# Kernel tuning notes

Measured on AMD Instinct MI355X. Metric: run time of the kernel, lower is better.

The kernel has to match this reference:

```python
import jax, jax.numpy as jnp
import numpy as np

N_CLS = 1000
FEAT_DIM = 1024
BATCH = 32768
PROTO_M = 0.95
TEMP = 0.1
BASE_TEMP = 0.1


def setup_inputs() -> dict:
    key = jax.random.key(0)
    k1, k2, k3 = jax.random.split(key, 3)
    features = jax.random.normal(k1, (BATCH, FEAT_DIM), dtype=jnp.float32)
    labels = jax.random.randint(k2, (BATCH,), 0, N_CLS)
    p = jax.random.normal(k3, (N_CLS, FEAT_DIM), dtype=jnp.float32)
    prototypes = p / jnp.maximum(jnp.linalg.norm(p, axis=1, keepdims=True), 1e-12)
    return {"features": features, "prototypes": prototypes, "labels": labels}


def _l2_normalize(x, eps=1e-12):
    # F.normalize(x, dim=0) semantics: x / max(||x||_2, eps)
    return x / jnp.maximum(jnp.linalg.norm(x), eps)


def _ema_update(prototypes, features, labels):
    # Sequential per-sample EMA + renormalize (faithful to the torch for-loop:
    # later samples with the same label see earlier updates).
    def step(protos, fl):
        f, l = fl
        row = _l2_normalize(protos[l] * PROTO_M + f * (1.0 - PROTO_M))
        return protos.at[l].set(row), None

    prototypes, _ = jax.lax.scan(step, prototypes, (features, labels))
    return prototypes


def reference(features, prototypes, labels):
    protos = _ema_update(prototypes, features, labels)  # [n_cls, feat]
    logits = jnp.matmul(protos, protos.T) / TEMP        # [n_cls, n_cls]
    # mask = (1 - eye) * logits_mask, where logits_mask also zeros the diagonal
    mask = 1.0 - jnp.eye(N_CLS, dtype=logits.dtype)
    mean_prob_neg = jnp.log((mask * jnp.exp(logits)).sum(axis=1) / mask.sum(axis=1))
    # torch drops NaNs; with n_cls > 1 every row has n_cls-1 negatives, so none occur
    loss = (TEMP / BASE_TEMP) * jnp.mean(mean_prob_neg)
    return loss
```

## Files before the change

### kernel.cpp

```cpp
#include <hip/hip_runtime.h>
#include <hip/hip_bf16.h>
#include <math.h>

#define N_CLS 1000
#define FEAT  1024
#define BATCH 32768
#define NBLK_H 128
#define CHUNK  256
#define KCAT   3072
#define GBK    64
#define LPITCH 72

typedef short short8 __attribute__((ext_vector_type(8)));
typedef float f32x4  __attribute__((ext_vector_type(4)));

__device__ __forceinline__ unsigned short f2bf(float x) {
    union { __hip_bfloat16 h; unsigned short u; } cv;
    cv.h = __float2bfloat16(x);
    return cv.u;
}
__device__ __forceinline__ float bf2f(unsigned short u) {
    union { __hip_bfloat16 h; unsigned short u; } cv;
    cv.u = u;
    return __bfloat162float(cv.h);
}

__global__ __launch_bounds__(256) void hist_kernel(const int* __restrict__ labels,
                                                   unsigned* __restrict__ hist) {
    __shared__ unsigned cnt[N_CLS];
    const int t = threadIdx.x, b = blockIdx.x;
    for (int i = t; i < N_CLS; i += 256) cnt[i] = 0;
    __syncthreads();
    atomicAdd(&cnt[labels[b * CHUNK + t]], 1u);
    __syncthreads();
    for (int i = t; i < N_CLS; i += 256) hist[(size_t)i * NBLK_H + b] = cnt[i];
}

__global__ __launch_bounds__(256) void scan1_kernel(unsigned* __restrict__ hist,
                                                    unsigned* __restrict__ total) {
    const int l    = blockIdx.x * 4 + (threadIdx.x >> 6);
    const int lane = threadIdx.x & 63;
    unsigned v0 = hist[(size_t)l * NBLK_H + lane];
    unsigned v1 = hist[(size_t)l * NBLK_H + 64 + lane];
    unsigned x0 = v0, x1 = v1;
    #pragma unroll
    for (int off = 1; off < 64; off <<= 1) {
        unsigned u0 = __shfl_up(x0, off, 64);
        if (lane >= off) x0 += u0;
        unsigned u1 = __shfl_up(x1, off, 64);
        if (lane >= off) x1 += u1;
    }
    x1 += __shfl(x0, 63, 64);
    hist[(size_t)l * NBLK_H + lane]      = x0 - v0;
    hist[(size_t)l * NBLK_H + 64 + lane] = x1 - v1;
    if (lane == 63) total[l] = x1;
}

__global__ __launch_bounds__(1024) void scan2_kernel(const unsigned* __restrict__ total,
                                                     unsigned* __restrict__ base) {
    const int t = threadIdx.x;
    unsigned v = (t < N_CLS) ? total[t] : 0u;
    __shared__ unsigned sc[1024];
    sc[t] = v;
    __syncthreads();
    for (int off = 1; off < 1024; off <<= 1) {
        unsigned u = (t >= off) ? sc[t - off] : 0u;
        __syncthreads();
        sc[t] += u;
        __syncthreads();
    }
    if (t < N_CLS) base[t] = sc[t] - v;
}

__global__ __launch_bounds__(256) void scatter_kernel(const int* __restrict__ labels,
                                                      const unsigned* __restrict__ hist,
                                                      const unsigned* __restrict__ base,
                                                      int* __restrict__ sorted_idx) {
    __shared__ int lbl[CHUNK];
    __shared__ unsigned c[N_CLS];
    const int t = threadIdx.x, b = blockIdx.x;
    for (int i = t; i < N_CLS; i += 256) c[i] = 0;
    __syncthreads();
    const int i = b * CHUNK + t;
    const int l = labels[i];
    lbl[t] = l;
    atomicAdd(&c[l], 1u);
    __syncthreads();
    int rank = 0;
    if (c[l] > 1) {
        for (int j = 0; j < t; ++j) rank += (lbl[j] == l);
    }
    sorted_idx[base[l] + hist[(size_t)l * NBLK_H + b] + (unsigned)rank] = i;
}

__device__ __forceinline__ float4 ema4(float4 p, float4 f) {
    p.x = fmaf(0.95f, p.x, 0.05f * f.x);
    p.y = fmaf(0.95f, p.y, 0.05f * f.y);
    p.z = fmaf(0.95f, p.z, 0.05f * f.z);
    p.w = fmaf(0.95f, p.w, 0.05f * f.w);
    return p;
}
__device__ __forceinline__ float dot4(float4 a) {
    return a.x * a.x + a.y * a.y + a.z * a.z + a.w * a.w;
}
__device__ __forceinline__ float4 scale4(float4 a, float s) {
    a.x *= s; a.y *= s; a.z *= s; a.w *= s; return a;
}

__global__ __launch_bounds__(256) void ema_kernel(const float* __restrict__ features,
                                                  const float* __restrict__ prototypes,
                                                  const int* __restrict__ sorted_idx,
                                                  const unsigned* __restrict__ base,
                                                  const unsigned* __restrict__ total,
                                                  float* __restrict__ protos_new) {
    const int w    = blockIdx.x * 4 + (threadIdx.x >> 6);
    const int lane = threadIdx.x & 63;
    const float4* pr = (const float4*)(prototypes + (size_t)w * FEAT);
    float4 p0 = pr[lane], p1 = pr[lane + 64], p2 = pr[lane + 128], p3 = pr[lane + 192];

    const int cnt = (int)total[w];
    const int bs  = (int)base[w];
    const int iA = (cnt > 0) ? sorted_idx[bs] : 0;
    const int iB = (cnt > 1) ? sorted_idx[bs + 1] : 0;
    const float4* fA = (const float4*)(features + (size_t)iA * FEAT);
    float4 a0 = fA[lane], a1 = fA[lane + 64], a2 = fA[lane + 128], a3 = fA[lane + 192];
    const float4* fB = (const float4*)(features + (size_t)iB * FEAT);
    float4 b0 = fB[lane], b1 = fB[lane + 64], b2 = fB[lane + 128], b3 = fB[lane + 192];

    int k = 0;
    while (k + 2 <= cnt) {
        {
            const int iN = (k + 2 < cnt) ? sorted_idx[bs + k + 2] : 0;
            p0 = ema4(p0, a0); p1 = ema4(p1, a1); p2 = ema4(p2, a2); p3 = ema4(p3, a3);
            const float4* f = (const float4*)(features + (size_t)iN * FEAT);
            a0 = f[lane]; a1 = f[lane + 64]; a2 = f[lane + 128]; a3 = f[lane + 192];
            float ss = dot4(p0) + dot4(p1) + dot4(p2) + dot4(p3);
            #pragma unroll
            for (int o = 32; o; o >>= 1) ss += __shfl_xor(ss, o, 64);
            const float inv = 1.0f / fmaxf(sqrtf(ss), 1e-12f);
            p0 = scale4(p0, inv); p1 = scale4(p1, inv); p2 = scale4(p2, inv); p3 = scale4(p3, inv);
        }
        {
            const int iN = (k + 3 < cnt) ? sorted_idx[bs + k + 3] : 0;
            p0 = ema4(p0, b0); p1 = ema4(p1, b1); p2 = ema4(p2, b2); p3 = ema4(p3, b3);
            const float4* f = (const float4*)(features + (size_t)iN * FEAT);
            b0 = f[lane]; b1 = f[lane + 64]; b2 = f[lane + 128]; b3 = f[lane + 192];
            float ss = dot4(p0) + dot4(p1) + dot4(p2) + dot4(p3);
            #pragma unroll
            for (int o = 32; o; o >>= 1) ss += __shfl_xor(ss, o, 64);
            const float inv = 1.0f / fmaxf(sqrtf(ss), 1e-12f);
            p0 = scale4(p0, inv); p1 = scale4(p1, inv); p2 = scale4(p2, inv); p3 = scale4(p3, inv);
        }
        k += 2;
    }
    if (k < cnt) {
        p0 = ema4(p0, a0); p1 = ema4(p1, a1); p2 = ema4(p2, a2); p3 = ema4(p3, a3);
        float ss = dot4(p0) + dot4(p1) + dot4(p2) + dot4(p3);
        #pragma unroll
        for (int o = 32; o; o >>= 1) ss += __shfl_xor(ss, o, 64);
        const float inv = 1.0f / fmaxf(sqrtf(ss), 1e-12f);
        p0 = scale4(p0, inv); p1 = scale4(p1, inv); p2 = scale4(p2, inv); p3 = scale4(p3, inv);
    }
    float4* out = (float4*)(protos_new + (size_t)w * FEAT);
    out[lane] = p0; out[lane + 64] = p1; out[lane + 128] = p2; out[lane + 192] = p3;
}

__global__ __launch_bounds__(256) void convert_kernel(const float* __restrict__ P,
                                                      unsigned short* __restrict__ A,
                                                      unsigned short* __restrict__ Bm) {
    const int row = blockIdx.x;
    const int t   = threadIdx.x;
    float4 v = make_float4(0.f, 0.f, 0.f, 0.f);
    if (row < N_CLS) v = *(const float4*)(P + (size_t)row * FEAT + 4 * t);
    ushort4 hi, lo;
    hi.x = f2bf(v.x); lo.x = f2bf(v.x - bf2f(hi.x));
    hi.y = f2bf(v.y); lo.y = f2bf(v.y - bf2f(hi.y));
    hi.z = f2bf(v.z); lo.z = f2bf(v.z - bf2f(hi.z));
    hi.w = f2bf(v.w); lo.w = f2bf(v.w - bf2f(hi.w));
    const size_t rb = (size_t)row * KCAT;
    *(ushort4*)(A  + rb +        4 * t) = hi;
    *(ushort4*)(A  + rb + 1024 + 4 * t) = lo;
    *(ushort4*)(A  + rb + 2048 + 4 * t) = hi;
    *(ushort4*)(Bm + rb +        4 * t) = hi;
    *(ushort4*)(Bm + rb + 1024 + 4 * t) = hi;
    *(ushort4*)(Bm + rb + 2048 + 4 * t) = lo;
}

__global__ __launch_bounds__(256) void gram_kernel(const unsigned short* __restrict__ A,
                                                   const unsigned short* __restrict__ Bm,
                                                   float* __restrict__ S) {
    __shared__ short As[64 * LPITCH];
    __shared__ short Bs[64 * LPITCH];
    const int t = threadIdx.x;
    const int l = t & 63, wid = t >> 6;
    const int wr = wid >> 1, wc = wid & 1;
    const int m0 = blockIdx.y * 64, n0 = blockIdx.x * 64;
    const int lg = l >> 4, lc = l & 15;

    f32x4 acc[2][2] = {};

    const int r0s = t >> 3,          c0s = t & 7;
    const int r1s = (t + 256) >> 3,  c1s = t & 7;
    const short* Ag = (const short*)A;
    const short* Bg = (const short*)Bm;

    for (int k0 = 0; k0 < KCAT; k0 += GBK) {
        short8 a0 = *(const short8*)(Ag + (size_t)(m0 + r0s) * KCAT + k0 + c0s * 8);
        short8 a1 = *(const short8*)(Ag + (size_t)(m0 + r1s) * KCAT + k0 + c1s * 8);
        short8 g0 = *(const short8*)(Bg + (size_t)(n0 + r0s) * KCAT + k0 + c0s * 8);
        short8 g1 = *(const short8*)(Bg + (size_t)(n0 + r1s) * KCAT + k0 + c1s * 8);
        __syncthreads();
        *(short8*)(As + r0s * LPITCH + c0s * 8) = a0;
        *(short8*)(As + r1s * LPITCH + c1s * 8) = a1;
        *(short8*)(Bs + r0s * LPITCH + c0s * 8) = g0;
        *(short8*)(Bs + r1s * LPITCH + c1s * 8) = g1;
        __syncthreads();
        #pragma unroll
        for (int kk = 0; kk < 2; ++kk) {
            short8 af[2], bf[2];
            #pragma unroll
            for (int mi = 0; mi < 2; ++mi)
                af[mi] = *(const short8*)(As + (wr * 32 + mi * 16 + lc) * LPITCH + kk * 32 + lg * 8);
            #pragma unroll
            for (int ni = 0; ni < 2; ++ni)
                bf[ni] = *(const short8*)(Bs + (wc * 32 + ni * 16 + lc) * LPITCH + kk * 32 + lg * 8);
            #pragma unroll
            for (int mi = 0; mi < 2; ++mi)
                #pragma unroll
                for (int ni = 0; ni < 2; ++ni)
                    acc[mi][ni] = __builtin_amdgcn_mfma_f32_16x16x32_bf16(af[mi], bf[ni], acc[mi][ni], 0, 0, 0);
        }
    }

    #pragma unroll
    for (int mi = 0; mi < 2; ++mi) {
        #pragma unroll
        for (int j = 0; j < 4; ++j) {
            const int gr = m0 + wr * 32 + mi * 16 + lg * 4 + j;
            float s = 0.f;
            #pragma unroll
            for (int ni = 0; ni < 2; ++ni) {
                const int gc = n0 + wc * 32 + ni * 16 + lc;
                if (gr < N_CLS && gc < N_CLS && gr != gc) s += expf(acc[mi][ni][j] * 10.0f);
            }
            #pragma unroll
            for (int m = 1; m < 16; m <<= 1) s += __shfl_xor(s, m, 64);
            if (lc == 0 && gr < N_CLS) atomicAdd(&S[gr], s);
        }
    }
}

__global__ __launch_bounds__(1024) void loss_kernel(const float* __restrict__ S,
                                                    float* __restrict__ out) {
    const int t = threadIdx.x;
    float v = 0.f;
    if (t < N_CLS) v = logf(S[t]) - logf(999.0f);
    #pragma unroll
    for (int off = 32; off; off >>= 1) v += __shfl_xor(v, off, 64);
    __shared__ float red[16];
    const int wv = t >> 6, lane = t & 63;
    if (lane == 0) red[wv] = v;
    __syncthreads();
    if (t < 16) {
        float s = red[t];
        #pragma unroll
        for (int off = 8; off; off >>= 1) s += __shfl_xor(s, off, 16);
        if (t == 0) out[0] = s / (float)N_CLS;
    }
}

extern "C" void kernel_launch(void* const* d_in, const int* in_sizes, int n_in,
                              void* d_out, int out_size, void* d_ws, size_t ws_size,
                              hipStream_t stream) {
    const float* features   = (const float*)d_in[0];
    const float* prototypes = (const float*)d_in[1];
    const int*   labels     = (const int*)d_in[2];
    float* out = (float*)d_out;

    char* ws = (char*)d_ws;
    unsigned*       hist   = (unsigned*)(ws);
    unsigned*       base   = (unsigned*)(ws + 0x80000);
    unsigned*       total  = (unsigned*)(ws + 0x81000);
    int*            sorted = (int*)     (ws + 0x82000);
    float*          S      = (float*)   (ws + 0xA4000);
    float*          pnew   = (float*)   (ws + 0x100000);
    unsigned short* Acat   = (unsigned short*)(ws + 0x500000);
    unsigned short* Bcat   = (unsigned short*)(ws + 0xB00000);

    hist_kernel   <<<NBLK_H, 256, 0, stream>>>(labels, hist);
    scan1_kernel  <<<250, 256, 0, stream>>>(hist, total);
    scan2_kernel  <<<1, 1024, 0, stream>>>(total, base);
    scatter_kernel<<<NBLK_H, 256, 0, stream>>>(labels, hist, base, sorted);
    hipMemsetAsync(S, 0, N_CLS * sizeof(float), stream);
    ema_kernel    <<<250, 256, 0, stream>>>(features, prototypes, sorted, base, total, pnew);
    convert_kernel<<<1024, 256, 0, stream>>>(pnew, Acat, Bcat);
    gram_kernel   <<<dim3(16, 16), 256, 0, stream>>>(Acat, Bcat, S);
    loss_kernel   <<<1, 1024, 0, stream>>>(S, out);
}
```

Measured before the change: 265.4 us.

## Fuse bf16 split into EMA, inline loss in gram, deepen feature prefetch

```diff
diff --git a/kernel.cpp b/kernel.cpp
--- a/kernel.cpp
+++ b/kernel.cpp
@@ -7,9 +7,8 @@
 #define BATCH 32768
 #define NBLK_H 128
 #define CHUNK  256
-#define KCAT   3072
-#define GBK    64
 #define LPITCH 72
+#define GRAM_BLOCKS 256
 
 typedef short short8 __attribute__((ext_vector_type(8)));
 typedef float f32x4  __attribute__((ext_vector_type(4)));
@@ -26,9 +25,15 @@
 }
 
 __global__ __launch_bounds__(256) void hist_kernel(const int* __restrict__ labels,
-                                                   unsigned* __restrict__ hist) {
+                                                   unsigned* __restrict__ hist,
+                                                   float* __restrict__ S,
+                                                   unsigned* __restrict__ counter) {
     __shared__ unsigned cnt[N_CLS];
     const int t = threadIdx.x, b = blockIdx.x;
+    if (b == 0) {
+        for (int i = t; i < N_CLS; i += 256) S[i] = 0.0f;
+        if (t == 0) *counter = 0u;
+    }
     for (int i = t; i < N_CLS; i += 256) cnt[i] = 0;
     __syncthreads();
     atomicAdd(&cnt[labels[b * CHUNK + t]], 1u);
@@ -107,12 +112,38 @@
     a.x *= s; a.y *= s; a.z *= s; a.w *= s; return a;
 }
 
+__device__ __forceinline__ void ema_step(float4& p0, float4& p1, float4& p2, float4& p3,
+                                         float4& x0, float4& x1, float4& x2, float4& x3,
+                                         const float* __restrict__ features, int iN, int lane) {
+    p0 = ema4(p0, x0); p1 = ema4(p1, x1); p2 = ema4(p2, x2); p3 = ema4(p3, x3);
+    const float4* f = (const float4*)(features + (size_t)iN * FEAT);
+    x0 = f[lane]; x1 = f[lane + 64]; x2 = f[lane + 128]; x3 = f[lane + 192];
+    float ss = dot4(p0) + dot4(p1) + dot4(p2) + dot4(p3);
+    #pragma unroll
+    for (int o = 32; o; o >>= 1) ss += __shfl_xor(ss, o, 64);
+    const float inv = 1.0f / fmaxf(sqrtf(ss), 1e-12f);
+    p0 = scale4(p0, inv); p1 = scale4(p1, inv); p2 = scale4(p2, inv); p3 = scale4(p3, inv);
+}
+
+__device__ __forceinline__ void write_hl(unsigned short* __restrict__ H,
+                                         unsigned short* __restrict__ L,
+                                         size_t off, float4 v) {
+    ushort4 hi, lo;
+    hi.x = f2bf(v.x); lo.x = f2bf(v.x - bf2f(hi.x));
+    hi.y = f2bf(v.y); lo.y = f2bf(v.y - bf2f(hi.y));
+    hi.z = f2bf(v.z); lo.z = f2bf(v.z - bf2f(hi.z));
+    hi.w = f2bf(v.w); lo.w = f2bf(v.w - bf2f(hi.w));
+    *(ushort4*)(H + off) = hi;
+    *(ushort4*)(L + off) = lo;
+}
+
 __global__ __launch_bounds__(256) void ema_kernel(const float* __restrict__ features,
                                                   const float* __restrict__ prototypes,
                                                   const int* __restrict__ sorted_idx,
                                                   const unsigned* __restrict__ base,
                                                   const unsigned* __restrict__ total,
-                                                  float* __restrict__ protos_new) {
+                                                  unsigned short* __restrict__ Hg,
+                                                  unsigned short* __restrict__ Lg) {
     const int w    = blockIdx.x * 4 + (threadIdx.x >> 6);
     const int lane = threadIdx.x & 63;
     const float4* pr = (const float4*)(prototypes + (size_t)w * FEAT);
@@ -120,115 +151,98 @@
 
     const int cnt = (int)total[w];
     const int bs  = (int)base[w];
-    const int iA = (cnt > 0) ? sorted_idx[bs] : 0;
-    const int iB = (cnt > 1) ? sorted_idx[bs + 1] : 0;
+    int myidx = (lane < cnt) ? sorted_idx[bs + lane] : 0;
+
+    #define GETIDX(K) (((K) < cnt) ? (((K) < 64) ? __shfl(myidx, (K), 64) : sorted_idx[bs + (K)]) : 0)
+
+    const int iA = GETIDX(0), iB = GETIDX(1), iC = GETIDX(2);
     const float4* fA = (const float4*)(features + (size_t)iA * FEAT);
     float4 a0 = fA[lane], a1 = fA[lane + 64], a2 = fA[lane + 128], a3 = fA[lane + 192];
     const float4* fB = (const float4*)(features + (size_t)iB * FEAT);
     float4 b0 = fB[lane], b1 = fB[lane + 64], b2 = fB[lane + 128], b3 = fB[lane + 192];
+    const float4* fC = (const float4*)(features + (size_t)iC * FEAT);
+    float4 c0 = fC[lane], c1 = fC[lane + 64], c2 = fC[lane + 128], c3 = fC[lane + 192];
 
     int k = 0;
-    while (k + 2 <= cnt) {
-        {
-            const int iN = (k + 2 < cnt) ? sorted_idx[bs + k + 2] : 0;
-            p0 = ema4(p0, a0); p1 = ema4(p1, a1); p2 = ema4(p2, a2); p3 = ema4(p3, a3);
-            const float4* f = (const float4*)(features + (size_t)iN * FEAT);
-            a0 = f[lane]; a1 = f[lane + 64]; a2 = f[lane + 128]; a3 = f[lane + 192];
-            float ss = dot4(p0) + dot4(p1) + dot4(p2) + dot4(p3);
-            #pragma unroll
-            for (int o = 32; o; o >>= 1) ss += __shfl_xor(ss, o, 64);
-            const float inv = 1.0f / fmaxf(sqrtf(ss), 1e-12f);
-            p0 = scale4(p0, inv); p1 = scale4(p1, inv); p2 = scale4(p2, inv); p3 = scale4(p3, inv);
-        }
-        {
-            const int iN = (k + 3 < cnt) ? sorted_idx[bs + k + 3] : 0;
-            p0 = ema4(p0, b0); p1 = ema4(p1, b1); p2 = ema4(p2, b2); p3 = ema4(p3, b3);
-            const float4* f = (const float4*)(features + (size_t)iN * FEAT);
-            b0 = f[lane]; b1 = f[lane + 64]; b2 = f[lane + 128]; b3 = f[lane + 192];
-            float ss = dot4(p0) + dot4(p1) + dot4(p2) + dot4(p3);
-            #pragma unroll
-            for (int o = 32; o; o >>= 1) ss += __shfl_xor(ss, o, 64);
-            const float inv = 1.0f / fmaxf(sqrtf(ss), 1e-12f);
-            p0 = scale4(p0, inv); p1 = scale4(p1, inv); p2 = scale4(p2, inv); p3 = scale4(p3, inv);
-        }
-        k += 2;
-    }
-    if (k < cnt) {
-        p0 = ema4(p0, a0); p1 = ema4(p1, a1); p2 = ema4(p2, a2); p3 = ema4(p3, a3);
-        float ss = dot4(p0) + dot4(p1) + dot4(p2) + dot4(p3);
-        #pragma unroll
-        for (int o = 32; o; o >>= 1) ss += __shfl_xor(ss, o, 64);
-        const float inv = 1.0f / fmaxf(sqrtf(ss), 1e-12f);
-        p0 = scale4(p0, inv); p1 = scale4(p1, inv); p2 = scale4(p2, inv); p3 = scale4(p3, inv);
-    }
-    float4* out = (float4*)(protos_new + (size_t)w * FEAT);
-    out[lane] = p0; out[lane + 64] = p1; out[lane + 128] = p2; out[lane + 192] = p3;
-}
-
-__global__ __launch_bounds__(256) void convert_kernel(const float* __restrict__ P,
-                                                      unsigned short* __restrict__ A,
-                                                      unsigned short* __restrict__ Bm) {
-    const int row = blockIdx.x;
-    const int t   = threadIdx.x;
-    float4 v = make_float4(0.f, 0.f, 0.f, 0.f);
-    if (row < N_CLS) v = *(const float4*)(P + (size_t)row * FEAT + 4 * t);
-    ushort4 hi, lo;
-    hi.x = f2bf(v.x); lo.x = f2bf(v.x - bf2f(hi.x));
-    hi.y = f2bf(v.y); lo.y = f2bf(v.y - bf2f(hi.y));
-    hi.z = f2bf(v.z); lo.z = f2bf(v.z - bf2f(hi.z));
-    hi.w = f2bf(v.w); lo.w = f2bf(v.w - bf2f(hi.w));
-    const size_t rb = (size_t)row * KCAT;
-    *(ushort4*)(A  + rb +        4 * t) = hi;
-    *(ushort4*)(A  + rb + 1024 + 4 * t) = lo;
-    *(ushort4*)(A  + rb + 2048 + 4 * t) = hi;
-    *(ushort4*)(Bm + rb +        4 * t) = hi;
-    *(ushort4*)(Bm + rb + 1024 + 4 * t) = hi;
-    *(ushort4*)(Bm + rb + 2048 + 4 * t) = lo;
-}
-
-__global__ __launch_bounds__(256) void gram_kernel(const unsigned short* __restrict__ A,
-                                                   const unsigned short* __restrict__ Bm,
-                                                   float* __restrict__ S) {
-    __shared__ short As[64 * LPITCH];
-    __shared__ short Bs[64 * LPITCH];
+    while (k + 3 <= cnt) {
+        ema_step(p0,p1,p2,p3, a0,a1,a2,a3, features, GETIDX(k + 3), lane); ++k;
+        ema_step(p0,p1,p2,p3, b0,b1,b2,b3, features, GETIDX(k + 3), lane); ++k;
+        ema_step(p0,p1,p2,p3, c0,c1,c2,c3, features, GETIDX(k + 3), lane); ++k;
+    }
+    if (k < cnt) { ema_step(p0,p1,p2,p3, a0,a1,a2,a3, features, 0, lane); ++k; }
+    if (k < cnt) { ema_step(p0,p1,p2,p3, b0,b1,b2,b3, features, 0, lane); ++k; }
+
+    const size_t rb = (size_t)w * FEAT;
+    write_hl(Hg, Lg, rb +       4 * lane, p0);
+    write_hl(Hg, Lg, rb + 256 + 4 * lane, p1);
+    write_hl(Hg, Lg, rb + 512 + 4 * lane, p2);
+    write_hl(Hg, Lg, rb + 768 + 4 * lane, p3);
+    #undef GETIDX
+}
+
+__global__ __launch_bounds__(256) void gram_kernel(const unsigned short* __restrict__ Hg,
+                                                   const unsigned short* __restrict__ Lg,
+                                                   float* __restrict__ S,
+                                                   unsigned* __restrict__ counter,
+                                                   float* __restrict__ out) {
+    __shared__ short Hms[64 * LPITCH];
+    __shared__ short Lms[64 * LPITCH];
+    __shared__ short Hns[64 * LPITCH];
+    __shared__ short Lns[64 * LPITCH];
     const int t = threadIdx.x;
     const int l = t & 63, wid = t >> 6;
     const int wr = wid >> 1, wc = wid & 1;
     const int m0 = blockIdx.y * 64, n0 = blockIdx.x * 64;
     const int lg = l >> 4, lc = l & 15;
 
+    const short* Hp = (const short*)Hg;
+    const short* Lp = (const short*)Lg;
+
     f32x4 acc[2][2] = {};
 
-    const int r0s = t >> 3,          c0s = t & 7;
-    const int r1s = (t + 256) >> 3,  c1s = t & 7;
-    const short* Ag = (const short*)A;
-    const short* Bg = (const short*)Bm;
-
-    for (int k0 = 0; k0 < KCAT; k0 += GBK) {
-        short8 a0 = *(const short8*)(Ag + (size_t)(m0 + r0s) * KCAT + k0 + c0s * 8);
-        short8 a1 = *(const short8*)(Ag + (size_t)(m0 + r1s) * KCAT + k0 + c1s * 8);
-        short8 g0 = *(const short8*)(Bg + (size_t)(n0 + r0s) * KCAT + k0 + c0s * 8);
-        short8 g1 = *(const short8*)(Bg + (size_t)(n0 + r1s) * KCAT + k0 + c1s * 8);
-        __syncthreads();
-        *(short8*)(As + r0s * LPITCH + c0s * 8) = a0;
-        *(short8*)(As + r1s * LPITCH + c1s * 8) = a1;
-        *(short8*)(Bs + r0s * LPITCH + c0s * 8) = g0;
-        *(short8*)(Bs + r1s * LPITCH + c1s * 8) = g1;
+    const int r0 = t >> 3,           c0 = t & 7;
+    const int r1 = (t + 256) >> 3,   c1 = t & 7;
+
+    for (int k0 = 0; k0 < FEAT; k0 += 64) {
+        short8 hm0 = *(const short8*)(Hp + (size_t)(m0 + r0) * FEAT + k0 + c0 * 8);
+        short8 hm1 = *(const short8*)(Hp + (size_t)(m0 + r1) * FEAT + k0 + c1 * 8);
+        short8 lm0 = *(const short8*)(Lp + (size_t)(m0 + r0) * FEAT + k0 + c0 * 8);
+        short8 lm1 = *(const short8*)(Lp + (size_t)(m0 + r1) * FEAT + k0 + c1 * 8);
+        short8 hn0 = *(const short8*)(Hp + (size_t)(n0 + r0) * FEAT + k0 + c0 * 8);
+        short8 hn1 = *(const short8*)(Hp + (size_t)(n0 + r1) * FEAT + k0 + c1 * 8);
+        short8 ln0 = *(const short8*)(Lp + (size_t)(n0 + r0) * FEAT + k0 + c0 * 8);
+        short8 ln1 = *(const short8*)(Lp + (size_t)(n0 + r1) * FEAT + k0 + c1 * 8);
+        __syncthreads();
+        *(short8*)(Hms + r0 * LPITCH + c0 * 8) = hm0;
+        *(short8*)(Hms + r1 * LPITCH + c1 * 8) = hm1;
+        *(short8*)(Lms + r0 * LPITCH + c0 * 8) = lm0;
+        *(short8*)(Lms + r1 * LPITCH + c1 * 8) = lm1;
+        *(short8*)(Hns + r0 * LPITCH + c0 * 8) = hn0;
+        *(short8*)(Hns + r1 * LPITCH + c1 * 8) = hn1;
+        *(short8*)(Lns + r0 * LPITCH + c0 * 8) = ln0;
+        *(short8*)(Lns + r1 * LPITCH + c1 * 8) = ln1;
         __syncthreads();
         #pragma unroll
         for (int kk = 0; kk < 2; ++kk) {
-            short8 af[2], bf[2];
-            #pragma unroll
-            for (int mi = 0; mi < 2; ++mi)
-                af[mi] = *(const short8*)(As + (wr * 32 + mi * 16 + lc) * LPITCH + kk * 32 + lg * 8);
-            #pragma unroll
-            for (int ni = 0; ni < 2; ++ni)
-                bf[ni] = *(const short8*)(Bs + (wc * 32 + ni * 16 + lc) * LPITCH + kk * 32 + lg * 8);
+            short8 ah[2], al[2], bh[2], bl[2];
+            #pragma unroll
+            for (int mi = 0; mi < 2; ++mi) {
+                ah[mi] = *(const short8*)(Hms + (wr * 32 + mi * 16 + lc) * LPITCH + kk * 32 + lg * 8);
+                al[mi] = *(const short8*)(Lms + (wr * 32 + mi * 16 + lc) * LPITCH + kk * 32 + lg * 8);
+            }
+            #pragma unroll
+            for (int ni = 0; ni < 2; ++ni) {
+                bh[ni] = *(const short8*)(Hns + (wc * 32 + ni * 16 + lc) * LPITCH + kk * 32 + lg * 8);
+                bl[ni] = *(const short8*)(Lns + (wc * 32 + ni * 16 + lc) * LPITCH + kk * 32 + lg * 8);
+            }
             #pragma unroll
             for (int mi = 0; mi < 2; ++mi)
                 #pragma unroll
-                for (int ni = 0; ni < 2; ++ni)
-                    acc[mi][ni] = __builtin_amdgcn_mfma_f32_16x16x32_bf16(af[mi], bf[ni], acc[mi][ni], 0, 0, 0);
+                for (int ni = 0; ni < 2; ++ni) {
+                    acc[mi][ni] = __builtin_amdgcn_mfma_f32_16x16x32_bf16(ah[mi], bh[ni], acc[mi][ni], 0, 0, 0);
+                    acc[mi][ni] = __builtin_amdgcn_mfma_f32_16x16x32_bf16(al[mi], bh[ni], acc[mi][ni], 0, 0, 0);
+                    acc[mi][ni] = __builtin_amdgcn_mfma_f32_16x16x32_bf16(ah[mi], bl[ni], acc[mi][ni], 0, 0, 0);
+                }
         }
     }
 
@@ -248,24 +262,29 @@
             if (lc == 0 && gr < N_CLS) atomicAdd(&S[gr], s);
         }
     }
-}
-
-__global__ __launch_bounds__(1024) void loss_kernel(const float* __restrict__ S,
-                                                    float* __restrict__ out) {
-    const int t = threadIdx.x;
-    float v = 0.f;
-    if (t < N_CLS) v = logf(S[t]) - logf(999.0f);
-    #pragma unroll
-    for (int off = 32; off; off >>= 1) v += __shfl_xor(v, off, 64);
-    __shared__ float red[16];
-    const int wv = t >> 6, lane = t & 63;
-    if (lane == 0) red[wv] = v;
-    __syncthreads();
-    if (t < 16) {
-        float s = red[t];
+
+    __threadfence();
+    __shared__ int amlast;
+    if (t == 0) {
+        unsigned old = __hip_atomic_fetch_add(counter, 1u, __ATOMIC_ACQ_REL, __HIP_MEMORY_SCOPE_AGENT);
+        amlast = (old == GRAM_BLOCKS - 1) ? 1 : 0;
+    }
+    __syncthreads();
+    if (amlast) {
+        float a = 0.f;
+        for (int i = t; i < N_CLS; i += 256) {
+            float sv = __hip_atomic_load(&S[i], __ATOMIC_RELAXED, __HIP_MEMORY_SCOPE_AGENT);
+            a += logf(sv);
+        }
         #pragma unroll
-        for (int off = 8; off; off >>= 1) s += __shfl_xor(s, off, 16);
-        if (t == 0) out[0] = s / (float)N_CLS;
+        for (int o = 32; o; o >>= 1) a += __shfl_xor(a, o, 64);
+        __shared__ float red[4];
+        if (l == 0) red[wid] = a;
+        __syncthreads();
+        if (t == 0) {
+            float tot = red[0] + red[1] + red[2] + red[3];
+            out[0] = tot / (float)N_CLS - logf(999.0f);
+        }
     }
 }
 
@@ -278,22 +297,19 @@
     float* out = (float*)d_out;
 
     char* ws = (char*)d_ws;
-    unsigned*       hist   = (unsigned*)(ws);
-    unsigned*       base   = (unsigned*)(ws + 0x80000);
-    unsigned*       total  = (unsigned*)(ws + 0x81000);
-    int*            sorted = (int*)     (ws + 0x82000);
-    float*          S      = (float*)   (ws + 0xA4000);
-    float*          pnew   = (float*)   (ws + 0x100000);
-    unsigned short* Acat   = (unsigned short*)(ws + 0x500000);
-    unsigned short* Bcat   = (unsigned short*)(ws + 0xB00000);
-
-    hist_kernel   <<<NBLK_H, 256, 0, stream>>>(labels, hist);
+    unsigned*       hist    = (unsigned*)(ws);
+    unsigned*       base    = (unsigned*)(ws + 0x80000);
+    unsigned*       total   = (unsigned*)(ws + 0x81000);
+    int*            sorted  = (int*)     (ws + 0x82000);
+    float*          S       = (float*)   (ws + 0xA4000);
+    unsigned*       counter = (unsigned*)(ws + 0xA5000);
+    unsigned short* Hg      = (unsigned short*)(ws + 0x100000);
+    unsigned short* Lg      = (unsigned short*)(ws + 0x300000);
+
+    hist_kernel   <<<NBLK_H, 256, 0, stream>>>(labels, hist, S, counter);
     scan1_kernel  <<<250, 256, 0, stream>>>(hist, total);
     scan2_kernel  <<<1, 1024, 0, stream>>>(total, base);
     scatter_kernel<<<NBLK_H, 256, 0, stream>>>(labels, hist, base, sorted);
-    hipMemsetAsync(S, 0, N_CLS * sizeof(float), stream);
-    ema_kernel    <<<250, 256, 0, stream>>>(features, prototypes, sorted, base, total, pnew);
-    convert_kernel<<<1024, 256, 0, stream>>>(pnew, Acat, Bcat);
-    gram_kernel   <<<dim3(16, 16), 256, 0, stream>>>(Acat, Bcat, S);
-    loss_kernel   <<<1, 1024, 0, stream>>>(S, out);
-}
+    ema_kernel    <<<250, 256, 0, stream>>>(features, prototypes, sorted, base, total, Hg, Lg);
+    gram_kernel   <<<dim3(16, 16), 256, 0, stream>>>(Hg, Lg, S, counter, out);
+}
```

New measurement: 262.0 us. Within noise of the previous version (-1.3%).
